# Optimization experiments

Hardware: AMD Instinct MI355X
Metric: run time of the kernel (lower is better)

## Reference

```python
import jax, jax.numpy as jnp
import numpy as np

RANK = 16
ALPHA = 32.0
SCALING = ALPHA / RANK
DROPOUT_P = 0.1
IN_F = 4096
OUT_F = 4096


def setup_inputs() -> dict:
    key = jax.random.key(0)
    k_x, k_a = jax.random.split(key, 2)
    x = jax.random.normal(k_x, (4, 4096, IN_F), dtype=jnp.float32)
    # lora_A init: randn * 0.02 ; lora_B init: zeros in torch, but use small randn
    # here so gradients/outputs are non-trivial for kernel correctness checks.
    lora_A = jax.random.normal(k_a, (RANK, IN_F), dtype=jnp.float32) * 0.02
    lora_B = jax.random.normal(jax.random.fold_in(key, 7), (OUT_F, RANK), dtype=jnp.float32) * 0.02
    return {"x": x, "lora_A": lora_A, "lora_B": lora_B}


def reference(x, lora_A, lora_B):
    # Faithful to torch: materialize W = (B @ A) * scaling, then y = x @ W^T
    W = (lora_B @ lora_A) * SCALING          # [out, in]
    y = jnp.einsum('bsi,oi->bso', x, W)      # F.linear
    # inverted dropout (training mode), deterministic key for reproducibility
    keep = 1.0 - DROPOUT_P
    mask = jax.random.bernoulli(jax.random.key(42), keep, y.shape)
    return jnp.where(mask, y / keep, 0.0).astype(y.dtype)
```

## Files before the change

### kernel.cpp

```cpp
#include <hip/hip_runtime.h>
#include <stdint.h>


#define M_TOTAL 16384
#define IN_F 4096
#define OUT_F 4096

__device__ __forceinline__ uint32_t tf_bits(uint32_t idx) {
  const uint32_t ks0 = 0u;
  const uint32_t ks1 = 42u;
  const uint32_t ks2 = 0u ^ 42u ^ 0x1BD11BDAu;
  uint32_t x0 = 0u + ks0;
  uint32_t x1 = idx + ks1;
#define TFR(r) { x0 += x1; x1 = (x1 << (r)) | (x1 >> (32 - (r))); x1 ^= x0; }
  TFR(13) TFR(15) TFR(26) TFR(6)   x0 += ks1; x1 += ks2 + 1u;
  TFR(17) TFR(29) TFR(16) TFR(24)  x0 += ks2; x1 += ks0 + 2u;
  TFR(13) TFR(15) TFR(26) TFR(6)   x0 += ks0; x1 += ks1 + 3u;
  TFR(17) TFR(29) TFR(16) TFR(24)  x0 += ks1; x1 += ks2 + 4u;
  TFR(13) TFR(15) TFR(26) TFR(6)   x0 += ks2; x1 += ks0 + 5u;
#undef TFR
  return x0 ^ x1;
}

__device__ __forceinline__ float apply_dropout(float v, uint32_t idx) {
  uint32_t bits = tf_bits(idx);
  float u = __uint_as_float((bits >> 9) | 0x3f800000u) - 1.0f;
  return (u < 0.9f) ? v * (1.0f / 0.9f) : 0.0f;
}

__global__ __launch_bounds__(256) void lora_xa_kernel(
    const float* __restrict__ x, const float* __restrict__ A,
    float* __restrict__ t) {
  const int tid = threadIdx.x;
  const int row_in_blk = tid >> 4;
  const int chunk = tid & 15;
  const int m = blockIdx.x * 16 + row_in_blk;

  const float4* x4 = (const float4*)(x + (size_t)m * IN_F);
  const float4* A4 = (const float4*)A;

  float acc[16];
#pragma unroll
  for (int r = 0; r < 16; ++r) acc[r] = 0.0f;

  for (int j = 0; j < 64; ++j) {
    const int f4 = chunk + j * 16;
    const float4 xv = x4[f4];
#pragma unroll
    for (int r = 0; r < 16; ++r) {
      const float4 av = A4[r * 1024 + f4];
      acc[r] += xv.x * av.x + xv.y * av.y + xv.z * av.z + xv.w * av.w;
    }
  }

#pragma unroll
  for (int off = 1; off < 16; off <<= 1) {
#pragma unroll
    for (int r = 0; r < 16; ++r) acc[r] += __shfl_xor(acc[r], off, 64);
  }

  float out = acc[0];
#pragma unroll
  for (int r = 1; r < 16; ++r) out = (chunk == r) ? acc[r] : out;
  t[(size_t)m * 16 + chunk] = out * 2.0f;
}

__global__ __launch_bounds__(256) void lora_tb_kernel(
    const float* __restrict__ t, const float* __restrict__ B,
    float* __restrict__ y) {
  __shared__ float ts[64 * 16];
  const int tid = threadIdx.x;
  const int colblk = blockIdx.x & 3;
  const int rowblk = blockIdx.x >> 2;
  const int m0 = rowblk * 64;
  const int o = colblk * 1024 + tid * 4;

  ((float4*)ts)[tid] = ((const float4*)(t + (size_t)m0 * 16))[tid];

  float4 b[4][4];
#pragma unroll
  for (int c = 0; c < 4; ++c) {
#pragma unroll
    for (int q = 0; q < 4; ++q)
      b[c][q] = ((const float4*)(B + (size_t)(o + c) * 16))[q];
  }
  __syncthreads();

  for (int mi = 0; mi < 64; ++mi) {
    const int m = m0 + mi;
    float tr[16];
#pragma unroll
    for (int r = 0; r < 16; ++r) tr[r] = ts[mi * 16 + r];

    float accv[4];
#pragma unroll
    for (int c = 0; c < 4; ++c) {
      float s = 0.0f;
#pragma unroll
      for (int q = 0; q < 4; ++q) {
        const float4 bb = b[c][q];
        s += tr[4 * q + 0] * bb.x + tr[4 * q + 1] * bb.y +
             tr[4 * q + 2] * bb.z + tr[4 * q + 3] * bb.w;
      }
      accv[c] = s;
    }

    const uint32_t base = (uint32_t)m * (uint32_t)OUT_F + (uint32_t)o;
    float4 res;
    res.x = apply_dropout(accv[0], base + 0u);
    res.y = apply_dropout(accv[1], base + 1u);
    res.z = apply_dropout(accv[2], base + 2u);
    res.w = apply_dropout(accv[3], base + 3u);
    ((float4*)y)[((size_t)m * OUT_F + o) >> 2] = res;
  }
}

extern "C" void kernel_launch(void* const* d_in, const int* in_sizes, int n_in,
                              void* d_out, int out_size, void* d_ws, size_t ws_size,
                              hipStream_t stream) {
  const float* x = (const float*)d_in[0];
  const float* A = (const float*)d_in[1];
  const float* B = (const float*)d_in[2];
  float* y = (float*)d_out;
  float* t = (float*)d_ws;

  lora_xa_kernel<<<M_TOTAL / 16, 256, 0, stream>>>(x, A, t);
  lora_tb_kernel<<<(M_TOTAL / 64) * (OUT_F / 1024), 256, 0, stream>>>(t, B, y);
}
```

Measured before the change: 683.4 us.

## Register-block four rows per thread in x@A and simplify dropout mask test

The x@A kernel now has each 32-lane group handle four rows at once, so every loaded A vector is reused across four x rows and the reduction spans 32 lanes. The 1/0.9 dropout scale is folded into the t scaling, and the keep test becomes an integer compare on the raw threefry bits, removing the float conversion and multiply per output. The second kernel's row loop is unrolled by two. Costs are higher register pressure (64 accumulators) and possible rounding differences from moving the scale earlier.

```diff
diff --git a/kernel.cpp b/kernel.cpp
--- a/kernel.cpp
+++ b/kernel.cpp
@@ -22,47 +22,60 @@
   return x0 ^ x1;
 }
 
-__device__ __forceinline__ float apply_dropout(float v, uint32_t idx) {
-  uint32_t bits = tf_bits(idx);
-  float u = __uint_as_float((bits >> 9) | 0x3f800000u) - 1.0f;
-  return (u < 0.9f) ? v * (1.0f / 0.9f) : 0.0f;
-}
-
-__global__ __launch_bounds__(256) void lora_xa_kernel(
+__global__ __launch_bounds__(256, 2) void lora_xa_kernel(
     const float* __restrict__ x, const float* __restrict__ A,
     float* __restrict__ t) {
   const int tid = threadIdx.x;
-  const int row_in_blk = tid >> 4;
-  const int chunk = tid & 15;
-  const int m = blockIdx.x * 16 + row_in_blk;
+  const int g = tid >> 5;
+  const int c = tid & 31;
+  const int m0 = blockIdx.x * 32 + g * 4;
 
-  const float4* x4 = (const float4*)(x + (size_t)m * IN_F);
   const float4* A4 = (const float4*)A;
+  const float4* xr0 = (const float4*)x + (size_t)m0 * 1024;
 
-  float acc[16];
+  float acc[4][16];
 #pragma unroll
-  for (int r = 0; r < 16; ++r) acc[r] = 0.0f;
+  for (int tt = 0; tt < 4; ++tt)
+#pragma unroll
+    for (int r = 0; r < 16; ++r) acc[tt][r] = 0.0f;
 
-  for (int j = 0; j < 64; ++j) {
-    const int f4 = chunk + j * 16;
-    const float4 xv = x4[f4];
+  for (int j = 0; j < 32; ++j) {
+    const int f4 = c + j * 32;
+    float4 xv[4];
+#pragma unroll
+    for (int tt = 0; tt < 4; ++tt) xv[tt] = xr0[tt * 1024 + f4];
 #pragma unroll
     for (int r = 0; r < 16; ++r) {
       const float4 av = A4[r * 1024 + f4];
-      acc[r] += xv.x * av.x + xv.y * av.y + xv.z * av.z + xv.w * av.w;
+#pragma unroll
+      for (int tt = 0; tt < 4; ++tt)
+        acc[tt][r] += xv[tt].x * av.x + xv[tt].y * av.y +
+                      xv[tt].z * av.z + xv[tt].w * av.w;
     }
   }
 
 #pragma unroll
-  for (int off = 1; off < 16; off <<= 1) {
+  for (int off = 1; off <= 16; off <<= 1)
 #pragma unroll
-    for (int r = 0; r < 16; ++r) acc[r] += __shfl_xor(acc[r], off, 64);
+    for (int tt = 0; tt < 4; ++tt)
+#pragma unroll
+      for (int r = 0; r < 16; ++r)
+        acc[tt][r] += __shfl_xor(acc[tt][r], off, 64);
+
+  const int rr = c & 15;
+  float s[4];
+#pragma unroll
+  for (int tt = 0; tt < 4; ++tt) {
+    float v = acc[tt][0];
+#pragma unroll
+    for (int r = 1; r < 16; ++r) v = (rr == r) ? acc[tt][r] : v;
+    s[tt] = v;
   }
-
-  float out = acc[0];
-#pragma unroll
-  for (int r = 1; r < 16; ++r) out = (chunk == r) ? acc[r] : out;
-  t[(size_t)m * 16 + chunk] = out * 2.0f;
+  const bool hi = (c >= 16);
+  const float scale = 2.0f / 0.9f;
+  const int mrow = m0 + (hi ? 2 : 0);
+  t[(size_t)mrow * 16 + rr]       = (hi ? s[2] : s[0]) * scale;
+  t[(size_t)(mrow + 1) * 16 + rr] = (hi ? s[3] : s[1]) * scale;
 }
 
 __global__ __launch_bounds__(256) void lora_tb_kernel(
@@ -86,6 +99,7 @@
   }
   __syncthreads();
 
+#pragma unroll 2
   for (int mi = 0; mi < 64; ++mi) {
     const int m = m0 + mi;
     float tr[16];
@@ -107,10 +121,10 @@
 
     const uint32_t base = (uint32_t)m * (uint32_t)OUT_F + (uint32_t)o;
     float4 res;
-    res.x = apply_dropout(accv[0], base + 0u);
-    res.y = apply_dropout(accv[1], base + 1u);
-    res.z = apply_dropout(accv[2], base + 2u);
-    res.w = apply_dropout(accv[3], base + 3u);
+    res.x = (tf_bits(base + 0u) < 0xE6666600u) ? accv[0] : 0.0f;
+    res.y = (tf_bits(base + 1u) < 0xE6666600u) ? accv[1] : 0.0f;
+    res.z = (tf_bits(base + 2u) < 0xE6666600u) ? accv[2] : 0.0f;
+    res.w = (tf_bits(base + 3u) < 0xE6666600u) ? accv[3] : 0.0f;
     ((float4*)y)[((size_t)m * OUT_F + o) >> 2] = res;
   }
 }
@@ -124,6 +138,6 @@
   float* y = (float*)d_out;
   float* t = (float*)d_ws;
 
-  lora_xa_kernel<<<M_TOTAL / 16, 256, 0, stream>>>(x, A, t);
+  lora_xa_kernel<<<M_TOTAL / 32, 256, 0, stream>>>(x, A, t);
   lora_tb_kernel<<<(M_TOTAL / 64) * (OUT_F / 1024), 256, 0, stream>>>(t, B, y);
 }
```

Result: no change. 688.4 us (+0.7%).

## Fuse LoRA down- and up-projection into one kernel with shared-memory A tiles

Applied to the files above, without the earlier changes.

Merges the x·A and t·B kernels into a single kernel per 16-row block, keeping the rank-16 intermediate in shared memory instead of a workspace round-trip. A is staged through shared memory in chunks, the next x vector is prefetched, the dropout scale is folded into t, and the keep test becomes an integer threshold compare on the raw random bits. The fused kernel launches four times fewer blocks for the output phase and reloads B per 16 rows instead of per 64, which adds B traffic and may lower parallelism in the write-bound output stage.

```diff
diff --git a/kernel.cpp b/kernel.cpp
--- a/kernel.cpp
+++ b/kernel.cpp
@@ -22,96 +22,99 @@
   return x0 ^ x1;
 }
 
-__device__ __forceinline__ float apply_dropout(float v, uint32_t idx) {
-  uint32_t bits = tf_bits(idx);
-  float u = __uint_as_float((bits >> 9) | 0x3f800000u) - 1.0f;
-  return (u < 0.9f) ? v * (1.0f / 0.9f) : 0.0f;
-}
+__global__ __launch_bounds__(256, 4) void lora_fused_kernel(
+    const float* __restrict__ x, const float* __restrict__ A,
+    const float* __restrict__ B, float* __restrict__ y) {
+  __shared__ float4 As[16 * 128];
+  __shared__ float ts[16 * 16];
 
-__global__ __launch_bounds__(256) void lora_xa_kernel(
-    const float* __restrict__ x, const float* __restrict__ A,
-    float* __restrict__ t) {
   const int tid = threadIdx.x;
-  const int row_in_blk = tid >> 4;
-  const int chunk = tid & 15;
-  const int m = blockIdx.x * 16 + row_in_blk;
+  const int row = tid >> 4;
+  const int c = tid & 15;
+  const int m0 = blockIdx.x * 16;
 
-  const float4* x4 = (const float4*)(x + (size_t)m * IN_F);
+  const float4* x4 = (const float4*)x + (size_t)(m0 + row) * 1024;
   const float4* A4 = (const float4*)A;
 
   float acc[16];
 #pragma unroll
   for (int r = 0; r < 16; ++r) acc[r] = 0.0f;
 
-  for (int j = 0; j < 64; ++j) {
-    const int f4 = chunk + j * 16;
-    const float4 xv = x4[f4];
+  float4 xv = x4[c];
+
+  for (int ck = 0; ck < 8; ++ck) {
+    if (ck) __syncthreads();
 #pragma unroll
-    for (int r = 0; r < 16; ++r) {
-      const float4 av = A4[r * 1024 + f4];
-      acc[r] += xv.x * av.x + xv.y * av.y + xv.z * av.z + xv.w * av.w;
+    for (int i = 0; i < 8; ++i) {
+      const int idx = tid + i * 256;
+      const int r = idx >> 7, col = idx & 127;
+      As[r * 128 + col] = A4[r * 1024 + ck * 128 + col];
+    }
+    __syncthreads();
+
+#pragma unroll
+    for (int j = 0; j < 8; ++j) {
+      const int jj = ck * 8 + j;
+      const int jn = (jj + 1) & 63;
+      const float4 xn = x4[jn * 16 + c];
+
+#pragma unroll
+      for (int r = 0; r < 16; ++r) {
+        const float4 av = As[r * 128 + j * 16 + c];
+        acc[r] += xv.x * av.x + xv.y * av.y + xv.z * av.z + xv.w * av.w;
+      }
+      xv = xn;
     }
   }
 
 #pragma unroll
-  for (int off = 1; off < 16; off <<= 1) {
+  for (int off = 1; off < 16; off <<= 1)
 #pragma unroll
     for (int r = 0; r < 16; ++r) acc[r] += __shfl_xor(acc[r], off, 64);
-  }
 
   float out = acc[0];
 #pragma unroll
-  for (int r = 1; r < 16; ++r) out = (chunk == r) ? acc[r] : out;
-  t[(size_t)m * 16 + chunk] = out * 2.0f;
-}
-
-__global__ __launch_bounds__(256) void lora_tb_kernel(
-    const float* __restrict__ t, const float* __restrict__ B,
-    float* __restrict__ y) {
-  __shared__ float ts[64 * 16];
-  const int tid = threadIdx.x;
-  const int colblk = blockIdx.x & 3;
-  const int rowblk = blockIdx.x >> 2;
-  const int m0 = rowblk * 64;
-  const int o = colblk * 1024 + tid * 4;
-
-  ((float4*)ts)[tid] = ((const float4*)(t + (size_t)m0 * 16))[tid];
-
-  float4 b[4][4];
-#pragma unroll
-  for (int c = 0; c < 4; ++c) {
-#pragma unroll
-    for (int q = 0; q < 4; ++q)
-      b[c][q] = ((const float4*)(B + (size_t)(o + c) * 16))[q];
-  }
+  for (int r = 1; r < 16; ++r) out = (c == r) ? acc[r] : out;
+  ts[row * 16 + c] = out * (2.0f / 0.9f);
   __syncthreads();
 
-  for (int mi = 0; mi < 64; ++mi) {
-    const int m = m0 + mi;
-    float tr[16];
+  const float4* B4 = (const float4*)B;
+  float4* y4 = (float4*)y;
+
+  for (int cs = 0; cs < 4; ++cs) {
+    const int o = cs * 1024 + tid * 4;
+    float4 b[4][4];
 #pragma unroll
-    for (int r = 0; r < 16; ++r) tr[r] = ts[mi * 16 + r];
+    for (int cc = 0; cc < 4; ++cc)
+#pragma unroll
+      for (int q = 0; q < 4; ++q)
+        b[cc][q] = B4[(o + cc) * 4 + q];
 
-    float accv[4];
+    for (int mi = 0; mi < 16; ++mi) {
+      const float4* trow = (const float4*)&ts[mi * 16];
+      const float4 t0 = trow[0], t1 = trow[1], t2 = trow[2], t3 = trow[3];
+
+      float accv[4];
 #pragma unroll
-    for (int c = 0; c < 4; ++c) {
-      float s = 0.0f;
-#pragma unroll
-      for (int q = 0; q < 4; ++q) {
-        const float4 bb = b[c][q];
-        s += tr[4 * q + 0] * bb.x + tr[4 * q + 1] * bb.y +
-             tr[4 * q + 2] * bb.z + tr[4 * q + 3] * bb.w;
+      for (int cc = 0; cc < 4; ++cc) {
+        accv[cc] = t0.x * b[cc][0].x + t0.y * b[cc][0].y +
+                   t0.z * b[cc][0].z + t0.w * b[cc][0].w +
+                   t1.x * b[cc][1].x + t1.y * b[cc][1].y +
+                   t1.z * b[cc][1].z + t1.w * b[cc][1].w +
+                   t2.x * b[cc][2].x + t2.y * b[cc][2].y +
+                   t2.z * b[cc][2].z + t2.w * b[cc][2].w +
+                   t3.x * b[cc][3].x + t3.y * b[cc][3].y +
+                   t3.z * b[cc][3].z + t3.w * b[cc][3].w;
       }
-      accv[c] = s;
+
+      const uint32_t base = (uint32_t)(m0 + mi) * (uint32_t)OUT_F + (uint32_t)o;
+      float4 res;
+      res.x = (tf_bits(base + 0u) < 0xE6666600u) ? accv[0] : 0.0f;
+      res.y = (tf_bits(base + 1u) < 0xE6666600u) ? accv[1] : 0.0f;
+      res.z = (tf_bits(base + 2u) < 0xE6666600u) ? accv[2] : 0.0f;
+      res.w = (tf_bits(base + 3u) < 0xE6666600u) ? accv[3] : 0.0f;
+      y4[((size_t)(m0 + mi) * OUT_F + o) >> 2] = res;
     }
-
-    const uint32_t base = (uint32_t)m * (uint32_t)OUT_F + (uint32_t)o;
-    float4 res;
-    res.x = apply_dropout(accv[0], base + 0u);
-    res.y = apply_dropout(accv[1], base + 1u);
-    res.z = apply_dropout(accv[2], base + 2u);
-    res.w = apply_dropout(accv[3], base + 3u);
-    ((float4*)y)[((size_t)m * OUT_F + o) >> 2] = res;
   }
 }
 
@@ -122,8 +125,6 @@
   const float* A = (const float*)d_in[1];
   const float* B = (const float*)d_in[2];
   float* y = (float*)d_out;
-  float* t = (float*)d_ws;
 
-  lora_xa_kernel<<<M_TOTAL / 16, 256, 0, stream>>>(x, A, t);
-  lora_tb_kernel<<<(M_TOTAL / 64) * (OUT_F / 1024), 256, 0, stream>>>(t, B, y);
+  lora_fused_kernel<<<M_TOTAL / 16, 256, 0, stream>>>(x, A, B, y);
 }
```

Result: faster. 574.4 us (-15.9%).
